# Kernel tuning notes

Hardware: AMD Instinct MI355X
Metric: run time of the kernel (lower is better)

The kernel has to match this reference:

```python
import jax, jax.numpy as jnp
import numpy as np

N_LEVELS = 2 ** 4 - 1  # 4-bit uniform quantization -> 15 intervals


def fake_quant(x, lower, upper):
    """Uniform asymmetric fake-quantization with straight-through rounding.
    clamp to [lower, upper], quantize to 4-bit grid, dequantize."""
    scale = (upper - lower) / N_LEVELS
    xc = jnp.clip(x, lower, upper)
    q = (xc - lower) / scale
    # straight-through estimator for round
    q = q + jax.lax.stop_gradient(jnp.round(q) - q)
    return q * scale + lower


def setup_inputs() -> dict:
    key = jax.random.key(0)
    kA, kB = jax.random.split(key)
    A = jax.random.normal(kA, (128, 8, 256, 64), dtype=jnp.float32)
    B = jax.random.normal(kB, (128, 8, 64, 256), dtype=jnp.float32)
    # learnable per-tensor bounds (as found by init_quantization_scale search)
    a_lower = jnp.full((1,), -2.5, dtype=jnp.float32)
    a_upper = jnp.full((1,), 2.5, dtype=jnp.float32)
    b_lower = jnp.full((1,), -2.5, dtype=jnp.float32)
    b_upper = jnp.full((1,), 2.5, dtype=jnp.float32)
    return {"A": A, "B": B, "a_lower": a_lower, "a_upper": a_upper,
            "b_lower": b_lower, "b_upper": b_upper}


def reference(A, B, a_lower, a_upper, b_lower, b_upper):
    Aq = fake_quant(A, a_lower, a_upper)
    Bq = fake_quant(B, b_lower, b_upper)
    # batched matmul: [bw, h, n, d] @ [bw, h, d, n] -> [bw, h, n, n]
    return jnp.einsum('bhnd,bhdm->bhnm', Aq, Bq)
```

## Files before the change

kernel.cpp:

```cpp
#include <hip/hip_runtime.h>

typedef __attribute__((ext_vector_type(4))) int   int4v;
typedef __attribute__((ext_vector_type(4))) float float4v;

__device__ __forceinline__ int swz(int row, int slot) {
    return slot ^ ((row ^ (row >> 2)) & 3);
}

__device__ __forceinline__ int4v quant4(float4v v, float lo, float up,
                                        float scale, float inv) {
    float t0 = fminf(fmaxf(v[0], lo), up) - lo;
    float t1 = fminf(fmaxf(v[1], lo), up) - lo;
    float t2 = fminf(fmaxf(v[2], lo), up) - lo;
    float t3 = fminf(fmaxf(v[3], lo), up) - lo;
    float m0 = t0 * inv, m1 = t1 * inv, m2 = t2 * inv, m3 = t3 * inv;
    float r0 = rintf(m0), r1 = rintf(m1), r2 = rintf(m2), r3 = rintf(m3);
    float d0 = fabsf(fabsf(m0 - r0) - 0.5f);
    float d1 = fabsf(fabsf(m1 - r1) - 0.5f);
    float d2 = fabsf(fabsf(m2 - r2) - 0.5f);
    float d3 = fabsf(fabsf(m3 - r3) - 0.5f);
    if (fminf(fminf(d0, d1), fminf(d2, d3)) < 1e-4f) {
        r0 = rintf(t0 / scale); r1 = rintf(t1 / scale);
        r2 = rintf(t2 / scale); r3 = rintf(t3 / scale);
    }
    int4v q = {(int)r0, (int)r1, (int)r2, (int)r3};
    return q;
}

__device__ __forceinline__ unsigned bsum(int p) {
    return ((unsigned)p * 0x01010101u) >> 24;
}

__global__ __launch_bounds__(256, 4) void qmm_kernel(
    const float* __restrict__ A, const float* __restrict__ B,
    const float* __restrict__ aLo, const float* __restrict__ aUp,
    const float* __restrict__ bLo, const float* __restrict__ bUp,
    float* __restrict__ Out)
{
    __shared__ int   qA[256 * 16];
    __shared__ int   qB[256 * 16];
    __shared__ float RAf[256];
    __shared__ float CBf[256];

    const int tid = threadIdx.x;
    const int b   = blockIdx.x;

    const float lA = aLo[0], uA = aUp[0];
    const float lB = bLo[0], uB = bUp[0];
    const float sA  = (uA - lA) / 15.0f;
    const float sB  = (uB - lB) / 15.0f;
    const float iA  = 1.0f / sA;
    const float iB  = 1.0f / sB;
    const float sAB = sA * sB;

    const float4v* A4 = (const float4v*)(A + (size_t)b * 256 * 64);
    const float4v* B4 = (const float4v*)(B + (size_t)b * 64 * 256);
    float* outb = Out + (size_t)b * 256 * 256;

    #pragma unroll
    for (int it = 0; it < 16; ++it) {
        int f = it * 256 + tid;
        float4v v = A4[f];
        int4v q = quant4(v, lA, uA, sA, iA);
        int p  = q[0] | (q[1] << 8) | (q[2] << 16) | (q[3] << 24);
        int row = f >> 4, chunk = f & 15;
        qA[row * 16 + swz(row, chunk >> 2) * 4 + (chunk & 3)] = p;
    }

    const int u  = tid & 63;
    const int kg = tid >> 6;
    #pragma unroll
    for (int kb = 0; kb < 4; ++kb) {
        int k0 = kb * 16 + kg * 4;
        int4v q0 = quant4(B4[(size_t)(k0 + 0) * 64 + u], lB, uB, sB, iB);
        int4v q1 = quant4(B4[(size_t)(k0 + 1) * 64 + u], lB, uB, sB, iB);
        int4v q2 = quant4(B4[(size_t)(k0 + 2) * 64 + u], lB, uB, sB, iB);
        int4v q3 = quant4(B4[(size_t)(k0 + 3) * 64 + u], lB, uB, sB, iB);
        #pragma unroll
        for (int c = 0; c < 4; ++c) {
            int col = u * 4 + c;
            int p = q0[c] | (q1[c] << 8) | (q2[c] << 16) | (q3[c] << 24);
            qB[col * 16 + swz(col, kb) * 4 + kg] = p;
        }
    }

    __syncthreads();

    {
        unsigned sa = 0, sb = 0;
        #pragma unroll
        for (int j = 0; j < 16; ++j) {
            unsigned pa = (unsigned)qA[tid * 16 + swz(tid, j >> 2) * 4 + (j & 3)];
            unsigned pb = (unsigned)qB[tid * 16 + swz(tid, j >> 2) * 4 + (j & 3)];
            sa += bsum(pa);
            sb += bsum(pb);
        }
        float c32 = 32.0f * lA * lB;
        RAf[tid] = sA * lB * (float)sa + c32;
        CBf[tid] = lA * sB * (float)sb + c32;
    }
    __syncthreads();

    const int wave = tid >> 6, lane = tid & 63;
    const int lr = lane & 15;
    const int lk = lane >> 4;

    int4v afrag[4];
    #pragma unroll
    for (int rt = 0; rt < 4; ++rt) {
        int row = wave * 64 + rt * 16 + lr;
        afrag[rt] = *(const int4v*)&qA[row * 16 + swz(row, lk) * 4];
    }

    #pragma unroll 4
    for (int ct = 0; ct < 16; ++ct) {
        int col = ct * 16 + lr;
        int4v bfrag = *(const int4v*)&qB[col * 16 + swz(col, lk) * 4];
        float cb = CBf[col];
        #pragma unroll
        for (int rt = 0; rt < 4; ++rt) {
            int4v acc = {0, 0, 0, 0};
            acc = __builtin_amdgcn_mfma_i32_16x16x64_i8(afrag[rt], bfrag, acc, 0, 0, 0);
            int orow = wave * 64 + rt * 16 + lk * 4;
            #pragma unroll
            for (int r = 0; r < 4; ++r) {
                outb[(size_t)(orow + r) * 256 + col] =
                    sAB * (float)acc[r] + RAf[orow + r] + cb;
            }
        }
    }
}

extern "C" void kernel_launch(void* const* d_in, const int* in_sizes, int n_in,
                              void* d_out, int out_size, void* d_ws, size_t ws_size,
                              hipStream_t stream) {
    const float* A   = (const float*)d_in[0];
    const float* B   = (const float*)d_in[1];
    const float* aLo = (const float*)d_in[2];
    const float* aUp = (const float*)d_in[3];
    const float* bLo = (const float*)d_in[4];
    const float* bUp = (const float*)d_in[5];
    float* Out = (float*)d_out;

    int batches = in_sizes[0] / (256 * 64);
    qmm_kernel<<<batches, 256, 0, stream>>>(A, B, aLo, aUp, bLo, bUp, Out);
}
```

Baseline: 98.60 us.

## Split fused quantize+matmul into separate quant-pack and matmul-store kernels

Splits the single fused kernel into two launches. The first quantizes A and B to packed int8, computes the row and column correction sums, and writes everything to workspace. The second loads the packed fragments straight from global memory and runs the MFMA and output store without LDS or barriers, which frees LDS and should raise occupancy for the store-heavy phase. The cost is an extra kernel launch plus a global round trip for the packed data, which is small next to the 256x256 float output per batch. The fused kernel is kept as a fallback when the workspace is too small.

```diff
diff --git a/kernel.cpp b/kernel.cpp
--- a/kernel.cpp
+++ b/kernel.cpp
@@ -31,6 +31,131 @@
     return ((unsigned)p * 0x01010101u) >> 24;
 }
 
+__global__ __launch_bounds__(256, 4) void quant_pack_kernel(
+    const float* __restrict__ A, const float* __restrict__ B,
+    const float* __restrict__ aLo, const float* __restrict__ aUp,
+    const float* __restrict__ bLo, const float* __restrict__ bUp,
+    int4v* __restrict__ qAg, int4v* __restrict__ qBg,
+    float* __restrict__ RAg, float* __restrict__ CBg)
+{
+    __shared__ int qA[256 * 16];
+    __shared__ int qB[256 * 16];
+
+    const int tid = threadIdx.x;
+    const int b   = blockIdx.x;
+
+    const float lA = aLo[0], uA = aUp[0];
+    const float lB = bLo[0], uB = bUp[0];
+    const float sA = (uA - lA) / 15.0f;
+    const float sB = (uB - lB) / 15.0f;
+    const float iA = 1.0f / sA;
+    const float iB = 1.0f / sB;
+
+    const float4v* A4 = (const float4v*)(A + (size_t)b * 256 * 64);
+    const float4v* B4 = (const float4v*)(B + (size_t)b * 64 * 256);
+
+    #pragma unroll
+    for (int it = 0; it < 16; ++it) {
+        int f = it * 256 + tid;
+        float4v v = A4[f];
+        int4v q = quant4(v, lA, uA, sA, iA);
+        int p  = q[0] | (q[1] << 8) | (q[2] << 16) | (q[3] << 24);
+        int row = f >> 4, chunk = f & 15;
+        qA[row * 16 + swz(row, chunk >> 2) * 4 + (chunk & 3)] = p;
+    }
+
+    const int u  = tid & 63;
+    const int kg = tid >> 6;
+    #pragma unroll
+    for (int kb = 0; kb < 4; ++kb) {
+        int k0 = kb * 16 + kg * 4;
+        int4v q0 = quant4(B4[(size_t)(k0 + 0) * 64 + u], lB, uB, sB, iB);
+        int4v q1 = quant4(B4[(size_t)(k0 + 1) * 64 + u], lB, uB, sB, iB);
+        int4v q2 = quant4(B4[(size_t)(k0 + 2) * 64 + u], lB, uB, sB, iB);
+        int4v q3 = quant4(B4[(size_t)(k0 + 3) * 64 + u], lB, uB, sB, iB);
+        #pragma unroll
+        for (int c = 0; c < 4; ++c) {
+            int col = u * 4 + c;
+            int p = q0[c] | (q1[c] << 8) | (q2[c] << 16) | (q3[c] << 24);
+            qB[col * 16 + swz(col, kb) * 4 + kg] = p;
+        }
+    }
+
+    __syncthreads();
+
+    {
+        unsigned sa = 0, sb = 0;
+        #pragma unroll
+        for (int j = 0; j < 16; ++j) {
+            unsigned pa = (unsigned)qA[tid * 16 + swz(tid, j >> 2) * 4 + (j & 3)];
+            unsigned pb = (unsigned)qB[tid * 16 + swz(tid, j >> 2) * 4 + (j & 3)];
+            sa += bsum(pa);
+            sb += bsum(pb);
+        }
+        float c32 = 32.0f * lA * lB;
+        RAg[b * 256 + tid] = sA * lB * (float)sa + c32;
+        CBg[b * 256 + tid] = lA * sB * (float)sb + c32;
+    }
+
+    const int4v* qa4 = (const int4v*)qA;
+    const int4v* qb4 = (const int4v*)qB;
+    #pragma unroll
+    for (int i = 0; i < 4; ++i) {
+        qAg[(size_t)b * 1024 + i * 256 + tid] = qa4[i * 256 + tid];
+        qBg[(size_t)b * 1024 + i * 256 + tid] = qb4[i * 256 + tid];
+    }
+}
+
+__global__ __launch_bounds__(256, 4) void mm_store_kernel(
+    const int4v* __restrict__ qAg, const int4v* __restrict__ qBg,
+    const float* __restrict__ RAg, const float* __restrict__ CBg,
+    const float* __restrict__ aLo, const float* __restrict__ aUp,
+    const float* __restrict__ bLo, const float* __restrict__ bUp,
+    float* __restrict__ Out)
+{
+    const int tid = threadIdx.x;
+    const int b   = blockIdx.x;
+    const int lane = tid & 63, wave = tid >> 6;
+    const int lr = lane & 15, lk = lane >> 4;
+
+    const float sA  = (aUp[0] - aLo[0]) / 15.0f;
+    const float sB  = (bUp[0] - bLo[0]) / 15.0f;
+    const float sAB = sA * sB;
+
+    const int4v*   qa  = qAg + (size_t)b * 1024;
+    const int4v*   qb  = qBg + (size_t)b * 1024;
+    const float4v* ra4 = (const float4v*)(RAg + (size_t)b * 256);
+    const float*   cbp = CBg + (size_t)b * 256;
+    float* outb = Out + (size_t)b * 256 * 256;
+
+    int4v   afrag[4];
+    float4v RA[4];
+    #pragma unroll
+    for (int rt = 0; rt < 4; ++rt) {
+        int row = wave * 64 + rt * 16 + lr;
+        afrag[rt] = qa[row * 4 + swz(row, lk)];
+        RA[rt]    = ra4[wave * 16 + rt * 4 + lk];
+    }
+
+    const int4v z4 = {0, 0, 0, 0};
+    #pragma unroll 4
+    for (int ct = 0; ct < 16; ++ct) {
+        int col = ct * 16 + lr;
+        int4v bfrag = qb[col * 4 + swz(col, lk)];
+        float cb = cbp[col];
+        #pragma unroll
+        for (int rt = 0; rt < 4; ++rt) {
+            int4v acc = __builtin_amdgcn_mfma_i32_16x16x64_i8(afrag[rt], bfrag, z4, 0, 0, 0);
+            int orow = wave * 64 + rt * 16 + lk * 4;
+            #pragma unroll
+            for (int r = 0; r < 4; ++r) {
+                outb[(size_t)(orow + r) * 256 + col] =
+                    sAB * (float)acc[r] + RA[rt][r] + cb;
+            }
+        }
+    }
+}
+
 __global__ __launch_bounds__(256, 4) void qmm_kernel(
     const float* __restrict__ A, const float* __restrict__ B,
     const float* __restrict__ aLo, const float* __restrict__ aUp,
@@ -143,5 +268,19 @@
     float* Out = (float*)d_out;
 
     int batches = in_sizes[0] / (256 * 64);
-    qmm_kernel<<<batches, 256, 0, stream>>>(A, B, aLo, aUp, bLo, bUp, Out);
-}
+    size_t need = (size_t)batches * (16384u * 2 + 1024u * 2);
+
+    if (ws_size >= need) {
+        char* w = (char*)d_ws;
+        int4v* qAg = (int4v*)w;
+        int4v* qBg = (int4v*)(w + (size_t)batches * 16384);
+        float* RAg = (float*)(w + (size_t)batches * 32768);
+        float* CBg = (float*)(w + (size_t)batches * 32768 + (size_t)batches * 1024);
+        quant_pack_kernel<<<batches, 256, 0, stream>>>(A, B, aLo, aUp, bLo, bUp,
+                                                       qAg, qBg, RAg, CBg);
+        mm_store_kernel<<<batches, 256, 0, stream>>>(qAg, qBg, RAg, CBg,
+                                                     aLo, aUp, bLo, bUp, Out);
+    } else {
+        qmm_kernel<<<batches, 256, 0, stream>>>(A, B, aLo, aUp, bLo, bUp, Out);
+    }
+}
```

Result: slower. 176.2 us (+78.7%).

## Switch int8 MFMA from 16x16x64 to 32x32x32 tiles with wider column stores

Applied to the files above, without the earlier changes.

Replaces the 16x16x64 int8 MFMA tiling with 32x32x32 MFMA, accumulating two k-halves per 32x32 output tile, and restructures the output loop so each lane writes 32-column-wide rows. The row bias terms are preloaded per tile into registers and the epilogue uses fmaf. This aims to cut the number of MFMA and LDS fragment loads and to improve store coalescing (32 contiguous floats per row segment instead of 16). It changes register pressure and the instruction mix, and the kernel is likely bound by output writes.

```diff
diff --git a/kernel.cpp b/kernel.cpp
--- a/kernel.cpp
+++ b/kernel.cpp
@@ -1,7 +1,8 @@
 #include <hip/hip_runtime.h>
 
-typedef __attribute__((ext_vector_type(4))) int   int4v;
-typedef __attribute__((ext_vector_type(4))) float float4v;
+typedef __attribute__((ext_vector_type(4)))  int   int4v;
+typedef __attribute__((ext_vector_type(16))) int   int16v;
+typedef __attribute__((ext_vector_type(4)))  float float4v;
 
 __device__ __forceinline__ int swz(int row, int slot) {
     return slot ^ ((row ^ (row >> 2)) & 3);
@@ -101,31 +102,43 @@
     }
     __syncthreads();
 
-    const int wave = tid >> 6, lane = tid & 63;
-    const int lr = lane & 15;
-    const int lk = lane >> 4;
+    const int lane = tid & 63, wave = tid >> 6;
+    const int ln = lane & 31, h = lane >> 5;
 
-    int4v afrag[4];
+    const int4v* qA4 = (const int4v*)qA;
+    const int4v* qB4 = (const int4v*)qB;
+    const int16v z16 = {0,0,0,0,0,0,0,0,0,0,0,0,0,0,0,0};
+
     #pragma unroll
-    for (int rt = 0; rt < 4; ++rt) {
-        int row = wave * 64 + rt * 16 + lr;
-        afrag[rt] = *(const int4v*)&qA[row * 16 + swz(row, lk) * 4];
-    }
+    for (int tr = 0; tr < 2; ++tr) {
+        const int rbase = wave * 64 + tr * 32;
+        const int arow  = rbase + ln;
+        int4v af0 = qA4[arow * 4 + swz(arow, 0 + h)];
+        int4v af1 = qA4[arow * 4 + swz(arow, 2 + h)];
 
-    #pragma unroll 4
-    for (int ct = 0; ct < 16; ++ct) {
-        int col = ct * 16 + lr;
-        int4v bfrag = *(const int4v*)&qB[col * 16 + swz(col, lk) * 4];
-        float cb = CBf[col];
+        float4v RA[4];
         #pragma unroll
-        for (int rt = 0; rt < 4; ++rt) {
-            int4v acc = {0, 0, 0, 0};
-            acc = __builtin_amdgcn_mfma_i32_16x16x64_i8(afrag[rt], bfrag, acc, 0, 0, 0);
-            int orow = wave * 64 + rt * 16 + lk * 4;
+        for (int g = 0; g < 4; ++g)
+            RA[g] = *(const float4v*)&RAf[rbase + 8 * g + 4 * h];
+
+        #pragma unroll 2
+        for (int ct = 0; ct < 8; ++ct) {
+            const int col = ct * 32 + ln;
+            int4v bf0 = qB4[col * 4 + swz(col, 0 + h)];
+            int4v bf1 = qB4[col * 4 + swz(col, 2 + h)];
+            float cb  = CBf[col];
+
+            int16v acc = __builtin_amdgcn_mfma_i32_32x32x32_i8(af0, bf0, z16, 0, 0, 0);
+            acc        = __builtin_amdgcn_mfma_i32_32x32x32_i8(af1, bf1, acc, 0, 0, 0);
+
             #pragma unroll
-            for (int r = 0; r < 4; ++r) {
-                outb[(size_t)(orow + r) * 256 + col] =
-                    sAB * (float)acc[r] + RAf[orow + r] + cb;
+            for (int g = 0; g < 4; ++g) {
+                const int row0 = rbase + 8 * g + 4 * h;
+                #pragma unroll
+                for (int j = 0; j < 4; ++j) {
+                    outb[(size_t)(row0 + j) * 256 + col] =
+                        fmaf(sAB, (float)acc[g * 4 + j], RA[g][j] + cb);
+                }
             }
         }
     }
```

After: 101.9 us. 1.03x slower.
